# Kernel tuning notes

Hardware: AMD Instinct MI355X
Metric: run time of the kernel (lower is better)

The kernel has to match this reference:

```python
import jax, jax.numpy as jnp
import numpy as np

N = 50000

def gcn_conv(x, W, b, src, dst, n):
    # x: [N, Fin], W: [Fin, Fout]; PyG GCNConv: transform then sym-normalized aggregate (self-loops included in src/dst)
    h = x @ W  # [N, Fout]
    deg = jax.ops.segment_sum(jnp.ones_like(dst, dtype=h.dtype), dst, num_segments=n)
    inv_sqrt = jnp.where(deg > 0, jax.lax.rsqrt(deg), 0.0)
    norm = inv_sqrt[src] * inv_sqrt[dst]  # [E+N]
    msg = h[src] * norm[:, None]
    out = jax.ops.segment_sum(msg, dst, num_segments=n)
    return out + b


def setup_inputs() -> dict:
    key = jax.random.key(0)
    ks = jax.random.split(key, 8)
    d_in, d_h, n_exp, E = 64, 64, 16, 800000
    x = jax.random.normal(ks[0], (N, d_in), dtype=jnp.float32)
    edge_index = jax.random.randint(ks[1], (2, E), 0, N, dtype=jnp.int64)
    s = 1.0 / np.sqrt(d_in)
    W1 = jax.random.uniform(ks[2], (d_in, d_h), minval=-s, maxval=s, dtype=jnp.float32)
    b1 = jnp.zeros((d_h,), jnp.float32)
    W2 = jax.random.uniform(ks[3], (d_h, d_h), minval=-s, maxval=s, dtype=jnp.float32)
    b2 = jnp.zeros((d_h,), jnp.float32)
    Wc = jax.random.uniform(ks[4], (d_h, n_exp), minval=-s, maxval=s, dtype=jnp.float32)
    bc = jnp.zeros((n_exp,), jnp.float32)
    return {"x": x, "edge_index": edge_index, "W1": W1, "b1": b1, "W2": W2, "b2": b2, "Wc": Wc, "bc": bc}


def reference(x, edge_index, W1, b1, W2, b2, Wc, bc):
    # add self-loops once (PyG GCNConv default add_self_loops=True)
    loops = jnp.arange(N, dtype=edge_index.dtype)
    src = jnp.concatenate([edge_index[0], loops])
    dst = jnp.concatenate([edge_index[1], loops])
    h = jax.nn.relu(gcn_conv(x, W1, b1, src, dst, N))
    # dropout is identity in eval mode
    h = jax.nn.relu(gcn_conv(h, W2, b2, src, dst, N))
    return h @ Wc + bc
```

## Files before the change

kernel.cpp:

```cpp
#include <hip/hip_runtime.h>
#include <hip/hip_fp16.h>


#define FDIM 64
#define NCLS 16
#define TILE 2048

__global__ __launch_bounds__(256) void k_histgemm(const int* __restrict__ dst, int E,
                                                  int* __restrict__ H, int nblk,
                                                  const float* __restrict__ X,
                                                  const float* __restrict__ W,
                                                  __half* __restrict__ Yh, int n) {
    __shared__ float Ws[FDIM * FDIM];
    __shared__ int h[256];
    int t = threadIdx.x, blk = blockIdx.x;
    if (blk < nblk) {
        h[t] = 0;
        __syncthreads();
        int i0 = blk * TILE;
#pragma unroll
        for (int k = 0; k < TILE / 256; ++k) {
            int i = i0 + k * 256 + t;
            if (i < E) atomicAdd(&h[dst[i] >> 8], 1);
        }
        __syncthreads();
        H[blk * 256 + t] = h[t];
    } else {
        for (int i = t; i < FDIM * FDIM; i += 256) Ws[i] = W[i];
        __syncthreads();
        if (blk == nblk && t < 8)
            ((uint4*)Yh)[(size_t)n * 8 + t] = make_uint4(0, 0, 0, 0);
        int idx = (blk - nblk) * 256 + t;
        int row = idx >> 2;
        int cg = (idx & 3) * 16;
        if (row >= n) return;
        const float4* xr = (const float4*)(X + (size_t)row * FDIM);
        float4 xv[16];
#pragma unroll
        for (int i = 0; i < 16; ++i) xv[i] = xr[i];
        float acc[16];
#pragma unroll
        for (int c = 0; c < 16; ++c) acc[c] = 0.f;
#pragma unroll
        for (int i = 0; i < 16; ++i) {
            float xs[4] = {xv[i].x, xv[i].y, xv[i].z, xv[i].w};
#pragma unroll
            for (int j = 0; j < 4; ++j) {
                float xk = xs[j];
                const float* wr = &Ws[(i * 4 + j) * FDIM + cg];
#pragma unroll
                for (int c = 0; c < 16; ++c) acc[c] += xk * wr[c];
            }
        }
        unsigned u[8];
#pragma unroll
        for (int i = 0; i < 8; ++i) {
            __half2 hp = __floats2half2_rn(acc[2 * i], acc[2 * i + 1]);
            u[i] = *(unsigned*)&hp;
        }
        uint4* yo = (uint4*)(Yh + (size_t)row * FDIM + cg);
        yo[0] = make_uint4(u[0], u[1], u[2], u[3]);
        yo[1] = make_uint4(u[4], u[5], u[6], u[7]);
    }
}

__global__ __launch_bounds__(512) void k_scanH(int* __restrict__ H, int nblk, int* __restrict__ btot) {
    __shared__ int s[512];
    int t = threadIdx.x, b = blockIdx.x;
    int v = (t < nblk) ? H[t * 256 + b] : 0;
    s[t] = v;
    __syncthreads();
    for (int off = 1; off < 512; off <<= 1) {
        int add = (t >= off) ? s[t - off] : 0;
        __syncthreads();
        s[t] += add;
        __syncthreads();
    }
    if (t < nblk) H[t * 256 + b] = s[t] - v;
    if (t == 511) btot[b] = s[511];
}

__global__ __launch_bounds__(256) void k_scatA(const int* __restrict__ src, const int* __restrict__ dst,
                                               int E, const int* __restrict__ H,
                                               const int* __restrict__ btot, int nb,
                                               unsigned* __restrict__ tmp) {
    __shared__ int s[256];
    __shared__ int Hb[256];
    __shared__ int c2[256];
    int t = threadIdx.x, blk = blockIdx.x;
    int v = (t < nb) ? btot[t] : 0;
    s[t] = v;
    __syncthreads();
    for (int off = 1; off < 256; off <<= 1) {
        int add = (t >= off) ? s[t - off] : 0;
        __syncthreads();
        s[t] += add;
        __syncthreads();
    }
    Hb[t] = (s[t] - v) + H[blk * 256 + t];
    c2[t] = 0;
    __syncthreads();
    int i0 = blk * TILE;
#pragma unroll
    for (int k = 0; k < TILE / 256; ++k) {
        int i = i0 + k * 256 + t;
        if (i < E) {
            int sv = src[i], d = dst[i];
            int b = d >> 8;
            unsigned rec = ((unsigned)(d & 255) << 16) | (unsigned)sv;
            int pos = Hb[b] + atomicAdd(&c2[b], 1);
            tmp[pos] = rec;
        }
    }
}

#define COLCAP 8192
__global__ __launch_bounds__(256) void k_binB(const unsigned* __restrict__ tmp,
                                              const int* __restrict__ btot, int nb,
                                              int n, int E, int* __restrict__ row_ptr,
                                              float* __restrict__ inv,
                                              unsigned short* __restrict__ col) {
    __shared__ int dcnt[256], s[256], cur[256];
    __shared__ unsigned short colbuf[COLCAP];
    int t = threadIdx.x, b = blockIdx.x;
    int v = (t < nb) ? btot[t] : 0;
    s[t] = v;
    __syncthreads();
    for (int off = 1; off < 256; off <<= 1) {
        int add = (t >= off) ? s[t - off] : 0;
        __syncthreads();
        s[t] += add;
        __syncthreads();
    }
    __shared__ int baseS;
    if (t == b) baseS = s[t] - v;
    dcnt[t] = 0;
    __syncthreads();
    int base = baseS;
    int cntE = btot[b];
    int node0 = b << 8;
    int nn = min(256, n - node0);
    for (int i = t; i < cntE; i += 256) atomicAdd(&dcnt[tmp[base + i] >> 16], 1);
    __syncthreads();
    int deg = dcnt[t];
    s[t] = deg;
    __syncthreads();
    for (int off = 1; off < 256; off <<= 1) {
        int add = (t >= off) ? s[t - off] : 0;
        __syncthreads();
        s[t] += add;
        __syncthreads();
    }
    int excl = s[t] - deg;
    if (t < nn) {
        row_ptr[node0 + t] = base + excl;
        inv[node0 + t] = rsqrtf((float)(deg + 1));
    }
    if (b == 0 && t == 0) { row_ptr[n] = E; inv[n] = 0.f; }
    cur[t] = excl;
    __syncthreads();
    for (int i = t; i < cntE; i += 256) {
        unsigned r = tmp[base + i];
        int pos = atomicAdd(&cur[r >> 16], 1);
        unsigned short vv = (unsigned short)(r & 0xFFFFu);
        if (pos < COLCAP) colbuf[pos] = vv;
        else col[base + pos] = vv;
    }
    __syncthreads();
    int lim = min(cntE, COLCAP);
    for (int i = t; i < lim; i += 256) col[base + i] = colbuf[i];
}

__device__ __forceinline__ void unpack8(const uint4& q, float* f) {
    float2 f0 = __half22float2(*(const __half2*)&q.x);
    float2 f1 = __half22float2(*(const __half2*)&q.y);
    float2 f2 = __half22float2(*(const __half2*)&q.z);
    float2 f3 = __half22float2(*(const __half2*)&q.w);
    f[0] = f0.x; f[1] = f0.y; f[2] = f1.x; f[3] = f1.y;
    f[4] = f2.x; f[5] = f2.y; f[6] = f3.x; f[7] = f3.y;
}

__global__ __launch_bounds__(256, 6) void k_aggF1(const __half* __restrict__ Ph, const float* __restrict__ inv,
                                                  const int* __restrict__ row_ptr,
                                                  const unsigned short* __restrict__ col,
                                                  const float* __restrict__ bias,
                                                  const float* __restrict__ W2,
                                                  __half* __restrict__ P2, int n) {
    __shared__ float W2s[FDIM * FDIM];
    __shared__ float rbuf[32][FDIM + 1];
    int t0 = threadIdx.x;
    for (int i = t0; i < FDIM * FDIM; i += 256) W2s[i] = W2[i];
    if (blockIdx.x == 0 && t0 < 8)
        ((uint4*)P2)[(size_t)n * 8 + t0] = make_uint4(0, 0, 0, 0);
    int lane = t0 & 63;
    int sub = lane >> 3;
    int fl = lane & 7;
    int wid = t0 >> 6;
    int nl = wid * 8 + sub;
    int node = blockIdx.x * 32 + nl;
    bool alive = node < n;
    int nodeC = alive ? node : (n - 1);
    float iv = inv[nodeC];
    const uint4* Pq = (const uint4*)Ph;
    uint4 selfq = Pq[(size_t)nodeC * 8 + fl];
    float a[8], f[8];
    unpack8(selfq, f);
#pragma unroll
    for (int i = 0; i < 8; ++i) a[i] = iv * f[i];
    int s = row_ptr[nodeC];
    int e = alive ? row_ptr[nodeC + 1] : s;
    for (int j = s; j < e; j += 8) {
        int c[8];
        float wk[8];
        uint4 q[8];
#pragma unroll
        for (int k = 0; k < 8; ++k) {
            int jj = j + k;
            c[k] = (jj < e) ? (int)col[jj] : n;
        }
#pragma unroll
        for (int k = 0; k < 8; ++k) wk[k] = inv[c[k]];
#pragma unroll
        for (int k = 0; k < 8; ++k) q[k] = Pq[(size_t)c[k] * 8 + fl];
#pragma unroll
        for (int k = 0; k < 8; ++k) {
            unpack8(q[k], f);
#pragma unroll
            for (int i = 0; i < 8; ++i) a[i] = fmaf(wk[k], f[i], a[i]);
        }
    }
    float4 bb0 = ((const float4*)bias)[fl * 2];
    float4 bb1 = ((const float4*)bias)[fl * 2 + 1];
    float bbv[8] = {bb0.x, bb0.y, bb0.z, bb0.w, bb1.x, bb1.y, bb1.z, bb1.w};
#pragma unroll
    for (int i = 0; i < 8; ++i)
        rbuf[nl][fl * 8 + i] = fmaxf(fmaf(iv, a[i], bbv[i]), 0.f);
    __syncthreads();
    int nl2 = t0 >> 3;
    int cg = t0 & 7;
    int node2 = blockIdx.x * 32 + nl2;
    const float* rr = rbuf[nl2];
    float o[8];
#pragma unroll
    for (int i = 0; i < 8; ++i) o[i] = 0.f;
#pragma unroll
    for (int i = 0; i < FDIM; ++i) {
        float xk = rr[i];
        const float* wv = &W2s[i * FDIM + cg * 8];
#pragma unroll
        for (int c = 0; c < 8; ++c) o[c] = fmaf(xk, wv[c], o[c]);
    }
    if (node2 < n) {
        float iv2 = inv[node2];
        unsigned u[4];
#pragma unroll
        for (int i = 0; i < 4; ++i) {
            __half2 hp = __floats2half2_rn(o[2 * i] * iv2, o[2 * i + 1] * iv2);
            u[i] = *(unsigned*)&hp;
        }
        ((uint4*)P2)[(size_t)node2 * 8 + cg] = make_uint4(u[0], u[1], u[2], u[3]);
    }
}

__global__ __launch_bounds__(256, 6) void k_aggF2(const __half* __restrict__ Ph, const float* __restrict__ inv,
                                                  const int* __restrict__ row_ptr,
                                                  const unsigned short* __restrict__ col,
                                                  const float* __restrict__ bias,
                                                  const float* __restrict__ Wc, const float* __restrict__ bc,
                                                  float* __restrict__ out, int n) {
    __shared__ float WcT[NCLS * FDIM];
    int t0 = threadIdx.x;
    for (int i = t0; i < FDIM * NCLS; i += 256) {
        int c = i & 15, ff = i >> 4;
        WcT[c * FDIM + ff] = Wc[i];
    }
    __syncthreads();
    int lane = t0 & 63;
    int sub = lane >> 3;
    int fl = lane & 7;
    int wid = t0 >> 6;
    int node = blockIdx.x * 32 + wid * 8 + sub;
    bool alive = node < n;
    int nodeC = alive ? node : (n - 1);
    float iv = inv[nodeC];
    const uint4* Pq = (const uint4*)Ph;
    uint4 selfq = Pq[(size_t)nodeC * 8 + fl];
    float a[8], f[8];
    unpack8(selfq, a);
    int s = row_ptr[nodeC];
    int e = alive ? row_ptr[nodeC + 1] : s;
    for (int j = s; j < e; j += 8) {
        int c[8];
        uint4 q[8];
#pragma unroll
        for (int k = 0; k < 8; ++k) {
            int jj = j + k;
            c[k] = (jj < e) ? (int)col[jj] : n;
        }
#pragma unroll
        for (int k = 0; k < 8; ++k) q[k] = Pq[(size_t)c[k] * 8 + fl];
#pragma unroll
        for (int k = 0; k < 8; ++k) {
            unpack8(q[k], f);
#pragma unroll
            for (int i = 0; i < 8; ++i) a[i] += f[i];
        }
    }
    float4 bb0 = ((const float4*)bias)[fl * 2];
    float4 bb1 = ((const float4*)bias)[fl * 2 + 1];
    float bbv[8] = {bb0.x, bb0.y, bb0.z, bb0.w, bb1.x, bb1.y, bb1.z, bb1.w};
    float r[8];
#pragma unroll
    for (int i = 0; i < 8; ++i) r[i] = fmaxf(fmaf(iv, a[i], bbv[i]), 0.f);
    float part[NCLS];
#pragma unroll
    for (int c = 0; c < NCLS; ++c) {
        float4 wv0 = ((const float4*)(WcT + c * FDIM))[fl * 2];
        float4 wv1 = ((const float4*)(WcT + c * FDIM))[fl * 2 + 1];
        part[c] = r[0] * wv0.x;
        part[c] = fmaf(r[1], wv0.y, part[c]);
        part[c] = fmaf(r[2], wv0.z, part[c]);
        part[c] = fmaf(r[3], wv0.w, part[c]);
        part[c] = fmaf(r[4], wv1.x, part[c]);
        part[c] = fmaf(r[5], wv1.y, part[c]);
        part[c] = fmaf(r[6], wv1.z, part[c]);
        part[c] = fmaf(r[7], wv1.w, part[c]);
    }
#pragma unroll
    for (int m = 1; m < 8; m <<= 1) {
#pragma unroll
        for (int c = 0; c < NCLS; ++c) part[c] += __shfl_xor(part[c], m, 64);
    }
    if (alive && fl < 4) {
        float4 bb2 = ((const float4*)bc)[fl];
        float4 o = make_float4(part[fl * 4 + 0] + bb2.x, part[fl * 4 + 1] + bb2.y,
                               part[fl * 4 + 2] + bb2.z, part[fl * 4 + 3] + bb2.w);
        ((float4*)out)[(size_t)node * 4 + fl] = o;
    }
}

static inline size_t align256(size_t x) { return (x + 255) & ~(size_t)255; }

extern "C" void kernel_launch(void* const* d_in, const int* in_sizes, int n_in,
                              void* d_out, int out_size, void* d_ws, size_t ws_size,
                              hipStream_t stream) {
    const float* x  = (const float*)d_in[0];
    const int*   ei = (const int*)d_in[1];
    const float* W1 = (const float*)d_in[2];
    const float* b1 = (const float*)d_in[3];
    const float* W2 = (const float*)d_in[4];
    const float* b2 = (const float*)d_in[5];
    const float* Wc = (const float*)d_in[6];
    const float* bc = (const float*)d_in[7];
    float* out = (float*)d_out;

    const int n = in_sizes[0] / FDIM;
    const int E = in_sizes[1] / 2;
    const int* src = ei;
    const int* dst = ei + E;

    const int nb = (n + 255) >> 8;
    const int nblk = (E + TILE - 1) / TILE;

    char* w = (char*)d_ws;
    size_t off = 0;
    int* H = (int*)(w + off);        off = align256(off + (size_t)nblk * 256 * 4);
    int* btot = (int*)(w + off);     off = align256(off + 256 * 4);
    int* row_ptr = (int*)(w + off);  off = align256(off + (size_t)(n + 1) * 4);
    float* inv = (float*)(w + off);  off = align256(off + (size_t)(n + 1) * 4);
    unsigned* tmp = (unsigned*)(w + off);             off = align256(off + (size_t)E * 4);
    unsigned short* col = (unsigned short*)(w + off); off = align256(off + (size_t)(E + 8) * 2);
    __half* P1 = (__half*)(w + off); off = align256(off + (size_t)(n + 1) * FDIM * 2);
    __half* P2 = (__half*)(w + off); off = align256(off + (size_t)(n + 1) * FDIM * 2);
    (void)ws_size;

    const int nbG = (n * 4 + 255) / 256;
    const int nbA = (n + 31) / 32;

    k_histgemm<<<nblk + nbG, 256, 0, stream>>>(dst, E, H, nblk, x, W1, P1, n);
    k_scanH<<<nb, 512, 0, stream>>>(H, nblk, btot);
    k_scatA<<<nblk, 256, 0, stream>>>(src, dst, E, H, btot, nb, tmp);
    k_binB<<<nb, 256, 0, stream>>>(tmp, btot, nb, n, E, row_ptr, inv, col);

    k_aggF1<<<nbA, 256, 0, stream>>>(P1, inv, row_ptr, col, b1, W2, P2, n);
    k_aggF2<<<nbA, 256, 0, stream>>>(P2, inv, row_ptr, col, b2, Wc, bc, out, n);
}
```

Measured before the change: 173.6 us.

## Pad CSR rows to multiples of eight for vectorized column loads

Each node's neighbor list is padded to a multiple of 8 entries, filled with the dummy node index n, and each block's segment is 8-aligned. The padded degree is packed into the upper bits of row_ptr, so the aggregation kernels read one row_ptr value and fetch 8 column indices with a single 16-byte load, with no per-element bounds checks. This removes the scalar index loads and the second row_ptr read, at the cost of extra padded gathers of the zero row, a larger col buffer, and a padding loop in binB. Launch bounds are also relaxed from 6 to 4 waves per SIMD.

```diff
diff --git a/kernel.cpp b/kernel.cpp
--- a/kernel.cpp
+++ b/kernel.cpp
@@ -122,6 +122,7 @@
                                               unsigned short* __restrict__ col) {
     __shared__ int dcnt[256], s[256], cur[256];
     __shared__ unsigned short colbuf[COLCAP];
+    __shared__ int baseS;
     int t = threadIdx.x, b = blockIdx.x;
     int v = (t < nb) ? btot[t] : 0;
     s[t] = v;
@@ -132,18 +133,19 @@
         s[t] += add;
         __syncthreads();
     }
-    __shared__ int baseS;
     if (t == b) baseS = s[t] - v;
     dcnt[t] = 0;
     __syncthreads();
     int base = baseS;
+    int pbase = ((base + 7) & ~7) + b * 2056;
     int cntE = btot[b];
     int node0 = b << 8;
     int nn = min(256, n - node0);
     for (int i = t; i < cntE; i += 256) atomicAdd(&dcnt[tmp[base + i] >> 16], 1);
     __syncthreads();
     int deg = dcnt[t];
-    s[t] = deg;
+    int pdeg = (deg + 7) & ~7;
+    s[t] = pdeg;
     __syncthreads();
     for (int off = 1; off < 256; off <<= 1) {
         int add = (t >= off) ? s[t - off] : 0;
@@ -151,24 +153,32 @@
         s[t] += add;
         __syncthreads();
     }
-    int excl = s[t] - deg;
+    int pexcl = s[t] - pdeg;
+    int ptot = s[255];
     if (t < nn) {
-        row_ptr[node0 + t] = base + excl;
+        row_ptr[node0 + t] = (pbase + pexcl) | ((pdeg >> 3) << 22);
         inv[node0 + t] = rsqrtf((float)(deg + 1));
     }
-    if (b == 0 && t == 0) { row_ptr[n] = E; inv[n] = 0.f; }
-    cur[t] = excl;
+    if (b == 0 && t == 0) inv[n] = 0.f;
+    cur[t] = pexcl;
     __syncthreads();
     for (int i = t; i < cntE; i += 256) {
         unsigned r = tmp[base + i];
         int pos = atomicAdd(&cur[r >> 16], 1);
         unsigned short vv = (unsigned short)(r & 0xFFFFu);
         if (pos < COLCAP) colbuf[pos] = vv;
-        else col[base + pos] = vv;
-    }
-    __syncthreads();
-    int lim = min(cntE, COLCAP);
-    for (int i = t; i < lim; i += 256) col[base + i] = colbuf[i];
+        else col[pbase + pos] = vv;
+    }
+    if (t < nn) {
+        int p1 = pexcl + pdeg;
+        for (int p = pexcl + deg; p < p1; ++p) {
+            if (p < COLCAP) colbuf[p] = (unsigned short)n;
+            else col[pbase + p] = (unsigned short)n;
+        }
+    }
+    __syncthreads();
+    int lim = min(ptot, COLCAP);
+    for (int i = t; i < lim; i += 256) col[pbase + i] = colbuf[i];
 }
 
 __device__ __forceinline__ void unpack8(const uint4& q, float* f) {
@@ -180,7 +190,7 @@
     f[4] = f2.x; f[5] = f2.y; f[6] = f3.x; f[7] = f3.y;
 }
 
-__global__ __launch_bounds__(256, 6) void k_aggF1(const __half* __restrict__ Ph, const float* __restrict__ inv,
+__global__ __launch_bounds__(256, 4) void k_aggF1(const __half* __restrict__ Ph, const float* __restrict__ inv,
                                                   const int* __restrict__ row_ptr,
                                                   const unsigned short* __restrict__ col,
                                                   const float* __restrict__ bias,
@@ -207,19 +217,20 @@
     unpack8(selfq, f);
 #pragma unroll
     for (int i = 0; i < 8; ++i) a[i] = iv * f[i];
-    int s = row_ptr[nodeC];
-    int e = alive ? row_ptr[nodeC + 1] : s;
+    int v = row_ptr[nodeC];
+    int s = v & 0x3FFFFF;
+    int e = alive ? s + ((v >> 22) << 3) : s;
     for (int j = s; j < e; j += 8) {
+        uint4 cv = *(const uint4*)(col + j);
         int c[8];
+        c[0] = cv.x & 0xFFFF; c[1] = cv.x >> 16;
+        c[2] = cv.y & 0xFFFF; c[3] = cv.y >> 16;
+        c[4] = cv.z & 0xFFFF; c[5] = cv.z >> 16;
+        c[6] = cv.w & 0xFFFF; c[7] = cv.w >> 16;
         float wk[8];
+#pragma unroll
+        for (int k = 0; k < 8; ++k) wk[k] = inv[c[k]];
         uint4 q[8];
-#pragma unroll
-        for (int k = 0; k < 8; ++k) {
-            int jj = j + k;
-            c[k] = (jj < e) ? (int)col[jj] : n;
-        }
-#pragma unroll
-        for (int k = 0; k < 8; ++k) wk[k] = inv[c[k]];
 #pragma unroll
         for (int k = 0; k < 8; ++k) q[k] = Pq[(size_t)c[k] * 8 + fl];
 #pragma unroll
@@ -262,7 +273,7 @@
     }
 }
 
-__global__ __launch_bounds__(256, 6) void k_aggF2(const __half* __restrict__ Ph, const float* __restrict__ inv,
+__global__ __launch_bounds__(256, 4) void k_aggF2(const __half* __restrict__ Ph, const float* __restrict__ inv,
                                                   const int* __restrict__ row_ptr,
                                                   const unsigned short* __restrict__ col,
                                                   const float* __restrict__ bias,
@@ -287,16 +298,17 @@
     uint4 selfq = Pq[(size_t)nodeC * 8 + fl];
     float a[8], f[8];
     unpack8(selfq, a);
-    int s = row_ptr[nodeC];
-    int e = alive ? row_ptr[nodeC + 1] : s;
+    int v = row_ptr[nodeC];
+    int s = v & 0x3FFFFF;
+    int e = alive ? s + ((v >> 22) << 3) : s;
     for (int j = s; j < e; j += 8) {
+        uint4 cv = *(const uint4*)(col + j);
         int c[8];
+        c[0] = cv.x & 0xFFFF; c[1] = cv.x >> 16;
+        c[2] = cv.y & 0xFFFF; c[3] = cv.y >> 16;
+        c[4] = cv.z & 0xFFFF; c[5] = cv.z >> 16;
+        c[6] = cv.w & 0xFFFF; c[7] = cv.w >> 16;
         uint4 q[8];
-#pragma unroll
-        for (int k = 0; k < 8; ++k) {
-            int jj = j + k;
-            c[k] = (jj < e) ? (int)col[jj] : n;
-        }
 #pragma unroll
         for (int k = 0; k < 8; ++k) q[k] = Pq[(size_t)c[k] * 8 + fl];
 #pragma unroll
@@ -369,7 +381,7 @@
     int* row_ptr = (int*)(w + off);  off = align256(off + (size_t)(n + 1) * 4);
     float* inv = (float*)(w + off);  off = align256(off + (size_t)(n + 1) * 4);
     unsigned* tmp = (unsigned*)(w + off);             off = align256(off + (size_t)E * 4);
-    unsigned short* col = (unsigned short*)(w + off); off = align256(off + (size_t)(E + 8) * 2);
+    unsigned short* col = (unsigned short*)(w + off); off = align256(off + ((size_t)E + (size_t)nb * 2056 + 64) * 2);
     __half* P1 = (__half*)(w + off); off = align256(off + (size_t)(n + 1) * FDIM * 2);
     __half* P2 = (__half*)(w + off); off = align256(off + (size_t)(n + 1) * FDIM * 2);
     (void)ws_size;
```

New measurement: 156.5 us. 9.9% less time.
